# Kernel tuning notes

Hardware: AMD Instinct MI355X
Metric: run time of the kernel (lower is better)

The kernel has to match this reference:

```python
import jax, jax.numpy as jnp
import numpy as np

N_LAYERS = 200
KSIZE = 7
L_IN = 1388
FC_IN = 188   # 1388 - 200*6
FC_OUT = 91


def setup_inputs() -> dict:
    key = jax.random.key(0)
    k_x, k_w, k_b, k_fw, k_fb = jax.random.split(key, 5)
    B = 1024
    x = jax.random.normal(k_x, (B, L_IN), dtype=jnp.float32)
    # Conv1d(1,1,7) weights: torch default init U(-s, s) with s = 1/sqrt(in_ch*k) = 1/sqrt(7)
    s = 1.0 / np.sqrt(KSIZE)
    conv_w = jax.random.uniform(k_w, (N_LAYERS, KSIZE), dtype=jnp.float32, minval=-s, maxval=s)
    conv_b = jax.random.uniform(k_b, (N_LAYERS,), dtype=jnp.float32, minval=-s, maxval=s)
    sf = 1.0 / np.sqrt(FC_IN)
    fc_w = jax.random.uniform(k_fw, (FC_OUT, FC_IN), dtype=jnp.float32, minval=-sf, maxval=sf)
    fc_b = jax.random.uniform(k_fb, (FC_OUT,), dtype=jnp.float32, minval=-sf, maxval=sf)
    return {"x": x, "conv_w": conv_w, "conv_b": conv_b, "fc_w": fc_w, "fc_b": fc_b}


def _conv1(h, w, b):
    # h: [B, L]; cross-correlation with taps w[0..6], valid padding -> [B, L-6]
    L_out = h.shape[1] - (KSIZE - 1)
    acc = w[0] * h[:, 0:L_out]
    for k in range(1, KSIZE):
        acc = acc + w[k] * h[:, k:k + L_out]
    return acc + b


def reference(x, conv_w, conv_b, fc_w, fc_b):
    h = x  # unsqueeze(1) is implicit: single channel handled as [B, L]
    for i in range(N_LAYERS):
        h = _conv1(h, conv_w[i], conv_b[i])
        if i < N_LAYERS - 1:  # last ReLU was popped in the torch module
            h = jax.nn.relu(h)
    # Linear(188, 91) applied to the length dim, then Sigmoid; squeeze channel dim
    out = jax.nn.sigmoid(h @ fc_w.T + fc_b)  # [B, 91]
    return out
```

## Files before the change

### kernel.cpp

```cpp
#include <hip/hip_runtime.h>
#include <math.h>

#define N_LAYERS 200
#define KSIZE 7
#define L_IN 1388
#define FC_IN 188
#define FC_OUT 91
#define NT 128
#define NSTAGES 13

typedef float v2f __attribute__((ext_vector_type(2)));

constexpr int s_lo(int s)  { return 16 * s; }
constexpr int s_hi(int s)  { return (s < 12) ? 16 * s + 16 : N_LAYERS; }
constexpr int lin_(int s)  { return L_IN - 6 * s_lo(s); }
constexpr int lout_(int s) { return L_IN - 6 * s_hi(s); }
constexpr int cut_(int s)  { return lout_(s) / 2; }
constexpr int marg_(int s) { return 6 * (s_hi(s) - s_lo(s)); }
constexpr int s_R(int s) {
    const int a = cut_(s) + marg_(s);
    const int b = lin_(s) - cut_(s);
    const int m = (a > b) ? a : b;
    return (m + 63) / 64;
}
constexpr int s_Re(int s) { return (s_R(s) + 1) & ~1; }

__device__ __forceinline__ float dpp_next(float v) {
    return __int_as_float(
        __builtin_amdgcn_mov_dpp(__float_as_int(v), 0x130, 0xf, 0xf, true));
}
__device__ __forceinline__ v2f dpp_next2(v2f v) {
    v2f o; o.x = dpp_next(v.x); o.y = dpp_next(v.y); return o;
}

__device__ __forceinline__ v2f pk_fma(v2f a, v2f b, v2f c) {
    return __builtin_elementwise_fma(a, b, c);
}
__device__ __forceinline__ v2f pk_max0(v2f a) {
    return __builtin_elementwise_max(a, (v2f)(0.0f));
}

struct WG { v2f w2[28]; v2f b2[4]; };

__device__ __forceinline__ void load_wg(WG& wg, const v2f* wbuf2,
                                        const v2f* bbuf2, int g) {
#pragma unroll
    for (int t = 0; t < 28; ++t) wg.w2[t] = wbuf2[g * 28 + t];
#pragma unroll
    for (int j = 0; j < 4; ++j) wg.b2[j] = bbuf2[g * 4 + j];
}

template<int R, bool NR3>
__device__ __forceinline__ void run4(v2f (&r2)[6], const WG& wg) {
    constexpr int P = R / 2;
#pragma unroll
    for (int jj = 0; jj < 4; ++jj) {
        v2f h[3];
        {
            constexpr int L1 = (P < 3) ? P : 3;
            v2f l1[L1];
#pragma unroll
            for (int t = 0; t < L1; ++t) l1[t] = dpp_next2(r2[t]);
#pragma unroll
            for (int t = 0; t < L1; ++t) h[t] = l1[t];
            if constexpr (P == 2) h[2] = dpp_next2(l1[0]);
        }
        v2f M[P + 2];
#pragma unroll
        for (int j = 0; j < P + 2; ++j) {
            const v2f a = (j < P) ? r2[j] : h[j - P];
            const v2f b = (j + 1 < P) ? r2[j + 1] : h[j + 1 - P];
            v2f m; m.x = a.y; m.y = b.x;
            M[j] = m;
        }
        const bool relu = !(NR3 && jj == 3);
#pragma unroll
        for (int j = 0; j < P; ++j) {
            v2f acc = wg.b2[jj];
#pragma unroll
            for (int d = 0; d < KSIZE; ++d) {
                v2f src;
                if (d % 2 == 0) {
                    const int m = j + d / 2;
                    src = (m < P) ? r2[m] : h[m - P];
                } else {
                    src = M[j + (d - 1) / 2];
                }
                acc = pk_fma(wg.w2[jj * 7 + d], src, acc);
            }
            r2[j] = relu ? pk_max0(acc) : acc;
        }
    }
}

template<int R, bool FINAL>
__device__ __forceinline__ void run_stage_g(v2f (&r2)[6], WG& A,
        const v2f* wbuf2, const v2f* bbuf2, int g0, int g1) {
#pragma unroll 1
    for (int g = g0; g < g1; g += 2) {
        WG B;
        load_wg(B, wbuf2, bbuf2, (g + 1 < 50) ? g + 1 : 49);
        run4<R, false>(r2, A);
        load_wg(A, wbuf2, bbuf2, (g + 2 < 50) ? g + 2 : 49);
        run4<R, FINAL>(r2, B);
    }
}

template<int Ro, int Rn>
__device__ __forceinline__ void repack(v2f (&r2)[6], v2f* lbuf2,
                                       int lane, int wid,
                                       int cut_o, int lout_o, int cut_n)
{
    const int base2  = (wid ? cut_o : 0) / 2;
    const int bound2 = (wid ? lout_o : cut_o) / 2;
#pragma unroll
    for (int j = 0; j < Ro / 2; ++j) {
        const int pg = base2 + lane * (Ro / 2) + j;
        if (pg < bound2) lbuf2[pg] = r2[j];
    }
    __syncthreads();
    const int nb2 = (wid ? cut_n : 0) / 2;
#pragma unroll
    for (int j = 0; j < Rn / 2; ++j) r2[j] = lbuf2[nb2 + lane * (Rn / 2) + j];
    __syncthreads();
}

template<int S>
struct Chain {
    __device__ static __forceinline__ void run(v2f (&r2)[6], WG& A,
        const v2f* wbuf2, const v2f* bbuf2, v2f* lbuf2, int lane, int wid)
    {
        run_stage_g<s_Re(S), false>(r2, A, wbuf2, bbuf2, 4 * S, 4 * S + 4);
        repack<s_Re(S), s_Re(S + 1)>(r2, lbuf2, lane, wid,
                                     cut_(S), lout_(S), cut_(S + 1));
        Chain<S + 1>::run(r2, A, wbuf2, bbuf2, lbuf2, lane, wid);
    }
};

template<>
struct Chain<NSTAGES - 1> {
    __device__ static __forceinline__ void run(v2f (&r2)[6], WG& A,
        const v2f* wbuf2, const v2f* bbuf2, v2f* lbuf2, int lane, int wid)
    {
        constexpr int R = s_Re(NSTAGES - 1);
        run_stage_g<R, true>(r2, A, wbuf2, bbuf2, 48, 50);
        const int base2  = wid ? 47 : 0;
        const int bound2 = wid ? 94 : 47;
#pragma unroll
        for (int j = 0; j < R / 2; ++j) {
            const int pg = base2 + lane * (R / 2) + j;
            if (pg < bound2) lbuf2[pg] = r2[j];
        }
        __syncthreads();
    }
};

__global__ __launch_bounds__(NT, 2) void conv_chain_kernel(
    const float* __restrict__ x,
    const float* __restrict__ conv_w,
    const float* __restrict__ conv_b,
    const float* __restrict__ fc_w,
    const float* __restrict__ fc_b,
    float* __restrict__ out)
{
    __shared__ __align__(16) v2f lbuf2[688];
    __shared__ __align__(16) v2f wbuf2[N_LAYERS * KSIZE];
    __shared__ __align__(16) v2f bbuf2[N_LAYERS];

    const int row  = blockIdx.x;
    const int tid  = threadIdx.x;
    const int lane = tid & 63;
    const int wid  = tid >> 6;

    for (int i = tid; i < N_LAYERS * KSIZE; i += NT) {
        const float v = conv_w[i];
        v2f p; p.x = v; p.y = v; wbuf2[i] = p;
    }
    for (int i = tid; i < N_LAYERS; i += NT) {
        const float v = conv_b[i];
        v2f p; p.x = v; p.y = v; bbuf2[i] = p;
    }

    v2f r2[6];
    const float* xr = x + (size_t)row * L_IN;
    const int c0 = wid ? cut_(0) : 0;
#pragma unroll
    for (int j = 0; j < 6; ++j) {
        const int p = c0 + lane * 12 + 2 * j;
        v2f v;
        if (p + 1 < L_IN)      v = *(const v2f*)(xr + p);
        else if (p < L_IN)     { v.x = xr[p]; v.y = 0.0f; }
        else                   { v.x = 0.0f;  v.y = 0.0f; }
        r2[j] = v;
    }
    __syncthreads();

    WG A;
    load_wg(A, wbuf2, bbuf2, 0);

    Chain<0>::run(r2, A, wbuf2, bbuf2, lbuf2, lane, wid);

    if (tid < FC_OUT) {
        float acc = fc_b[tid];
        const float4* wp = (const float4*)(fc_w + tid * FC_IN);
        const float4* hp = (const float4*)lbuf2;
#pragma unroll 4
        for (int q = 0; q < FC_IN / 4; ++q) {
            const float4 hv = hp[q];
            const float4 wv = wp[q];
            acc = fmaf(wv.x, hv.x, acc);
            acc = fmaf(wv.y, hv.y, acc);
            acc = fmaf(wv.z, hv.z, acc);
            acc = fmaf(wv.w, hv.w, acc);
        }
        out[(size_t)row * FC_OUT + tid] = 1.0f / (1.0f + expf(-acc));
    }
}

extern "C" void kernel_launch(void* const* d_in, const int* in_sizes, int n_in,
                              void* d_out, int out_size, void* d_ws, size_t ws_size,
                              hipStream_t stream) {
    const float* x      = (const float*)d_in[0];
    const float* conv_w = (const float*)d_in[1];
    const float* conv_b = (const float*)d_in[2];
    const float* fc_w   = (const float*)d_in[3];
    const float* fc_b   = (const float*)d_in[4];
    float* outp = (float*)d_out;

    const int batch = in_sizes[0] / L_IN;
    conv_chain_kernel<<<batch, NT, 0, stream>>>(x, conv_w, conv_b, fc_w, fc_b, outp);
}
```

Baseline: 115.3 us.

## Split each row across four waves with scalar FMAs and packed weight buffer

Each row is now processed by four wavefronts (256 threads) instead of two, with each lane holding up to 7 scalar values rather than packed float2 pairs, so the per-lane serial conv chain is shorter. Weights and biases are stored interleaved in one shared buffer of 32 floats per 4-layer group and loaded as float4. Launch bounds request 4 blocks per SU-equivalent. It trades packed FMA throughput and more halo recomputation and barrier participants for more parallel waves per row and lower per-lane latency.

```diff
diff --git a/kernel.cpp b/kernel.cpp
--- a/kernel.cpp
+++ b/kernel.cpp
@@ -6,156 +6,120 @@
 #define L_IN 1388
 #define FC_IN 188
 #define FC_OUT 91
-#define NT 128
+#define NT 256
+#define NW 4
 #define NSTAGES 13
+#define NGROUPS 50
+#define LBUF_N 1352
 
-typedef float v2f __attribute__((ext_vector_type(2)));
-
-constexpr int s_lo(int s)  { return 16 * s; }
-constexpr int s_hi(int s)  { return (s < 12) ? 16 * s + 16 : N_LAYERS; }
-constexpr int lin_(int s)  { return L_IN - 6 * s_lo(s); }
-constexpr int lout_(int s) { return L_IN - 6 * s_hi(s); }
-constexpr int cut_(int s)  { return lout_(s) / 2; }
-constexpr int marg_(int s) { return 6 * (s_hi(s) - s_lo(s)); }
+constexpr int lin_(int s)  { return L_IN - 96 * s; }
+constexpr int lout_(int s) { return (s < 12) ? L_IN - 96 * (s + 1) : FC_IN; }
+constexpr int nlay_(int s) { return (s < 12) ? 16 : 8; }
 constexpr int s_R(int s) {
-    const int a = cut_(s) + marg_(s);
-    const int b = lin_(s) - cut_(s);
-    const int m = (a > b) ? a : b;
-    return (m + 63) / 64;
+    const int span = lout_(s) / 4 + 1 + 6 * nlay_(s);
+    return (span + 63) / 64;
 }
-constexpr int s_Re(int s) { return (s_R(s) + 1) & ~1; }
 
 __device__ __forceinline__ float dpp_next(float v) {
     return __int_as_float(
         __builtin_amdgcn_mov_dpp(__float_as_int(v), 0x130, 0xf, 0xf, true));
 }
-__device__ __forceinline__ v2f dpp_next2(v2f v) {
-    v2f o; o.x = dpp_next(v.x); o.y = dpp_next(v.y); return o;
-}
 
-__device__ __forceinline__ v2f pk_fma(v2f a, v2f b, v2f c) {
-    return __builtin_elementwise_fma(a, b, c);
-}
-__device__ __forceinline__ v2f pk_max0(v2f a) {
-    return __builtin_elementwise_max(a, (v2f)(0.0f));
-}
+struct __align__(16) WG { float w[32]; };
 
-struct WG { v2f w2[28]; v2f b2[4]; };
-
-__device__ __forceinline__ void load_wg(WG& wg, const v2f* wbuf2,
-                                        const v2f* bbuf2, int g) {
+__device__ __forceinline__ void load_wg(WG& wg, const float4* kb4, int g) {
 #pragma unroll
-    for (int t = 0; t < 28; ++t) wg.w2[t] = wbuf2[g * 28 + t];
-#pragma unroll
-    for (int j = 0; j < 4; ++j) wg.b2[j] = bbuf2[g * 4 + j];
+    for (int q = 0; q < 8; ++q)
+        *reinterpret_cast<float4*>(&wg.w[4 * q]) = kb4[g * 8 + q];
 }
 
 template<int R, bool NR3>
-__device__ __forceinline__ void run4(v2f (&r2)[6], const WG& wg) {
-    constexpr int P = R / 2;
+__device__ __forceinline__ void run4(float (&r)[7], const WG& wg) {
 #pragma unroll
     for (int jj = 0; jj < 4; ++jj) {
-        v2f h[3];
+        float h[6];
         {
-            constexpr int L1 = (P < 3) ? P : 3;
-            v2f l1[L1];
+            constexpr int H1 = (R < 6) ? R : 6;
 #pragma unroll
-            for (int t = 0; t < L1; ++t) l1[t] = dpp_next2(r2[t]);
+            for (int t = 0; t < H1; ++t) h[t] = dpp_next(r[t]);
 #pragma unroll
-            for (int t = 0; t < L1; ++t) h[t] = l1[t];
-            if constexpr (P == 2) h[2] = dpp_next2(l1[0]);
-        }
-        v2f M[P + 2];
-#pragma unroll
-        for (int j = 0; j < P + 2; ++j) {
-            const v2f a = (j < P) ? r2[j] : h[j - P];
-            const v2f b = (j + 1 < P) ? r2[j + 1] : h[j + 1 - P];
-            v2f m; m.x = a.y; m.y = b.x;
-            M[j] = m;
+            for (int t = H1; t < 6; ++t) h[t] = dpp_next(h[t - R]);
         }
         const bool relu = !(NR3 && jj == 3);
 #pragma unroll
-        for (int j = 0; j < P; ++j) {
-            v2f acc = wg.b2[jj];
+        for (int j = 0; j < R; ++j) {
+            float acc = wg.w[28 + jj];
 #pragma unroll
             for (int d = 0; d < KSIZE; ++d) {
-                v2f src;
-                if (d % 2 == 0) {
-                    const int m = j + d / 2;
-                    src = (m < P) ? r2[m] : h[m - P];
-                } else {
-                    src = M[j + (d - 1) / 2];
-                }
-                acc = pk_fma(wg.w2[jj * 7 + d], src, acc);
+                const int m = j + d;
+                const float src = (m < R) ? r[m] : h[m - R];
+                acc = fmaf(wg.w[jj * 7 + d], src, acc);
             }
-            r2[j] = relu ? pk_max0(acc) : acc;
+            r[j] = relu ? fmaxf(acc, 0.0f) : acc;
         }
     }
 }
 
 template<int R, bool FINAL>
-__device__ __forceinline__ void run_stage_g(v2f (&r2)[6], WG& A,
-        const v2f* wbuf2, const v2f* bbuf2, int g0, int g1) {
+__device__ __forceinline__ void run_stage_g(float (&r)[7], WG& A,
+        const float4* kb4, int g0, int g1) {
 #pragma unroll 1
     for (int g = g0; g < g1; g += 2) {
         WG B;
-        load_wg(B, wbuf2, bbuf2, (g + 1 < 50) ? g + 1 : 49);
-        run4<R, false>(r2, A);
-        load_wg(A, wbuf2, bbuf2, (g + 2 < 50) ? g + 2 : 49);
-        run4<R, FINAL>(r2, B);
+        load_wg(B, kb4, (g + 1 < NGROUPS) ? g + 1 : NGROUPS - 1);
+        run4<R, false>(r, A);
+        load_wg(A, kb4, (g + 2 < NGROUPS) ? g + 2 : NGROUPS - 1);
+        run4<R, FINAL>(r, B);
     }
 }
 
 template<int Ro, int Rn>
-__device__ __forceinline__ void repack(v2f (&r2)[6], v2f* lbuf2,
-                                       int lane, int wid,
-                                       int cut_o, int lout_o, int cut_n)
-{
-    const int base2  = (wid ? cut_o : 0) / 2;
-    const int bound2 = (wid ? lout_o : cut_o) / 2;
+__device__ __forceinline__ void repack(float (&r)[7], float* lbuf,
+                                       int lane, int co, int co1, int cn) {
 #pragma unroll
-    for (int j = 0; j < Ro / 2; ++j) {
-        const int pg = base2 + lane * (Ro / 2) + j;
-        if (pg < bound2) lbuf2[pg] = r2[j];
+    for (int j = 0; j < Ro; ++j) {
+        const int p = co + lane * Ro + j;
+        if (p < co1) lbuf[p] = r[j];
     }
     __syncthreads();
-    const int nb2 = (wid ? cut_n : 0) / 2;
 #pragma unroll
-    for (int j = 0; j < Rn / 2; ++j) r2[j] = lbuf2[nb2 + lane * (Rn / 2) + j];
+    for (int j = 0; j < Rn; ++j) r[j] = lbuf[cn + lane * Rn + j];
     __syncthreads();
 }
 
 template<int S>
 struct Chain {
-    __device__ static __forceinline__ void run(v2f (&r2)[6], WG& A,
-        const v2f* wbuf2, const v2f* bbuf2, v2f* lbuf2, int lane, int wid)
+    __device__ static __forceinline__ void run(float (&r)[7], WG& A,
+        const float4* kb4, float* lbuf, int lane, int wid)
     {
-        run_stage_g<s_Re(S), false>(r2, A, wbuf2, bbuf2, 4 * S, 4 * S + 4);
-        repack<s_Re(S), s_Re(S + 1)>(r2, lbuf2, lane, wid,
-                                     cut_(S), lout_(S), cut_(S + 1));
-        Chain<S + 1>::run(r2, A, wbuf2, bbuf2, lbuf2, lane, wid);
+        run_stage_g<s_R(S), false>(r, A, kb4, 4 * S, 4 * S + 4);
+        const int co  = (wid * lout_(S)) >> 2;
+        const int co1 = ((wid + 1) * lout_(S)) >> 2;
+        const int cn  = (wid * lout_(S + 1)) >> 2;
+        repack<s_R(S), s_R(S + 1)>(r, lbuf, lane, co, co1, cn);
+        Chain<S + 1>::run(r, A, kb4, lbuf, lane, wid);
     }
 };
 
 template<>
 struct Chain<NSTAGES - 1> {
-    __device__ static __forceinline__ void run(v2f (&r2)[6], WG& A,
-        const v2f* wbuf2, const v2f* bbuf2, v2f* lbuf2, int lane, int wid)
+    __device__ static __forceinline__ void run(float (&r)[7], WG& A,
+        const float4* kb4, float* lbuf, int lane, int wid)
     {
-        constexpr int R = s_Re(NSTAGES - 1);
-        run_stage_g<R, true>(r2, A, wbuf2, bbuf2, 48, 50);
-        const int base2  = wid ? 47 : 0;
-        const int bound2 = wid ? 94 : 47;
+        constexpr int R = s_R(NSTAGES - 1);
+        run_stage_g<R, true>(r, A, kb4, 48, 50);
+        const int co  = (wid * FC_IN) >> 2;
+        const int co1 = ((wid + 1) * FC_IN) >> 2;
 #pragma unroll
-        for (int j = 0; j < R / 2; ++j) {
-            const int pg = base2 + lane * (R / 2) + j;
-            if (pg < bound2) lbuf2[pg] = r2[j];
+        for (int j = 0; j < R; ++j) {
+            const int p = co + lane * R + j;
+            if (p < co1) lbuf[p] = r[j];
         }
         __syncthreads();
     }
 };
 
-__global__ __launch_bounds__(NT, 2) void conv_chain_kernel(
+__global__ __launch_bounds__(NT, 4) void conv_chain_kernel(
     const float* __restrict__ x,
     const float* __restrict__ conv_w,
     const float* __restrict__ conv_b,
@@ -163,47 +127,40 @@
     const float* __restrict__ fc_b,
     float* __restrict__ out)
 {
-    __shared__ __align__(16) v2f lbuf2[688];
-    __shared__ __align__(16) v2f wbuf2[N_LAYERS * KSIZE];
-    __shared__ __align__(16) v2f bbuf2[N_LAYERS];
+    __shared__ __align__(16) float lbuf[LBUF_N];
+    __shared__ __align__(16) float kbuf[NGROUPS * 32];
 
     const int row  = blockIdx.x;
     const int tid  = threadIdx.x;
     const int lane = tid & 63;
     const int wid  = tid >> 6;
 
-    for (int i = tid; i < N_LAYERS * KSIZE; i += NT) {
-        const float v = conv_w[i];
-        v2f p; p.x = v; p.y = v; wbuf2[i] = p;
+    for (int i = tid; i < NGROUPS * 32; i += NT) {
+        const int g = i >> 5, t = i & 31;
+        kbuf[i] = (t < 28) ? conv_w[g * 28 + t] : conv_b[g * 4 + (t - 28)];
     }
-    for (int i = tid; i < N_LAYERS; i += NT) {
-        const float v = conv_b[i];
-        v2f p; p.x = v; p.y = v; bbuf2[i] = p;
-    }
+    for (int i = tid; i < LBUF_N; i += NT) lbuf[i] = 0.0f;
 
-    v2f r2[6];
+    float r[7];
     const float* xr = x + (size_t)row * L_IN;
-    const int c0 = wid ? cut_(0) : 0;
+    const int c0 = (wid * lout_(0)) >> 2;
 #pragma unroll
-    for (int j = 0; j < 6; ++j) {
-        const int p = c0 + lane * 12 + 2 * j;
-        v2f v;
-        if (p + 1 < L_IN)      v = *(const v2f*)(xr + p);
-        else if (p < L_IN)     { v.x = xr[p]; v.y = 0.0f; }
-        else                   { v.x = 0.0f;  v.y = 0.0f; }
-        r2[j] = v;
+    for (int j = 0; j < 7; ++j) {
+        const int p = c0 + lane * 7 + j;
+        r[j] = (p < L_IN) ? xr[p] : 0.0f;
     }
     __syncthreads();
 
     WG A;
-    load_wg(A, wbuf2, bbuf2, 0);
+    const float4* kb4 = reinterpret_cast<const float4*>(kbuf);
+    load_wg(A, kb4, 0);
 
-    Chain<0>::run(r2, A, wbuf2, bbuf2, lbuf2, lane, wid);
+    Chain<0>::run(r, A, kb4, lbuf, lane, wid);
 
     if (tid < FC_OUT) {
         float acc = fc_b[tid];
         const float4* wp = (const float4*)(fc_w + tid * FC_IN);
-        const float4* hp = (const float4*)lbuf2;
+        const float4* hp = (const float4*)lbuf;
 #pragma unroll 4
         for (int q = 0; q < FC_IN / 4; ++q) {
             const float4 hv = hp[q];
```

Result: slower. 132.6 us (+15.0%).

## Process two batch rows per block with 256 threads sharing weight LDS

Applied to the files above, without the earlier changes.

Each block now handles two rows using four waves (two per row), with separate LDS repack buffers per row, and launches half as many blocks. This amortizes the per-block weight/bias staging into shared memory across two rows and halves block count. In exchange, the block-wide syncthreads now couple two rows, so their stalls overlap less freely. Launch bounds stay at (NT,2), which may raise register pressure limits and change occupancy. Batch must be even.

```diff
diff --git a/kernel.cpp b/kernel.cpp
--- a/kernel.cpp
+++ b/kernel.cpp
@@ -6,7 +6,7 @@
 #define L_IN 1388
 #define FC_IN 188
 #define FC_OUT 91
-#define NT 128
+#define NT 256
 #define NSTAGES 13
 
 typedef float v2f __attribute__((ext_vector_type(2)));
@@ -108,18 +108,18 @@
 
 template<int Ro, int Rn>
 __device__ __forceinline__ void repack(v2f (&r2)[6], v2f* lbuf2,
-                                       int lane, int wid,
+                                       int lane, int rwid,
                                        int cut_o, int lout_o, int cut_n)
 {
-    const int base2  = (wid ? cut_o : 0) / 2;
-    const int bound2 = (wid ? lout_o : cut_o) / 2;
+    const int base2  = (rwid ? cut_o : 0) / 2;
+    const int bound2 = (rwid ? lout_o : cut_o) / 2;
 #pragma unroll
     for (int j = 0; j < Ro / 2; ++j) {
         const int pg = base2 + lane * (Ro / 2) + j;
         if (pg < bound2) lbuf2[pg] = r2[j];
     }
     __syncthreads();
-    const int nb2 = (wid ? cut_n : 0) / 2;
+    const int nb2 = (rwid ? cut_n : 0) / 2;
 #pragma unroll
     for (int j = 0; j < Rn / 2; ++j) r2[j] = lbuf2[nb2 + lane * (Rn / 2) + j];
     __syncthreads();
@@ -128,24 +128,24 @@
 template<int S>
 struct Chain {
     __device__ static __forceinline__ void run(v2f (&r2)[6], WG& A,
-        const v2f* wbuf2, const v2f* bbuf2, v2f* lbuf2, int lane, int wid)
+        const v2f* wbuf2, const v2f* bbuf2, v2f* lbuf2, int lane, int rwid)
     {
         run_stage_g<s_Re(S), false>(r2, A, wbuf2, bbuf2, 4 * S, 4 * S + 4);
-        repack<s_Re(S), s_Re(S + 1)>(r2, lbuf2, lane, wid,
+        repack<s_Re(S), s_Re(S + 1)>(r2, lbuf2, lane, rwid,
                                      cut_(S), lout_(S), cut_(S + 1));
-        Chain<S + 1>::run(r2, A, wbuf2, bbuf2, lbuf2, lane, wid);
+        Chain<S + 1>::run(r2, A, wbuf2, bbuf2, lbuf2, lane, rwid);
     }
 };
 
 template<>
 struct Chain<NSTAGES - 1> {
     __device__ static __forceinline__ void run(v2f (&r2)[6], WG& A,
-        const v2f* wbuf2, const v2f* bbuf2, v2f* lbuf2, int lane, int wid)
+        const v2f* wbuf2, const v2f* bbuf2, v2f* lbuf2, int lane, int rwid)
     {
         constexpr int R = s_Re(NSTAGES - 1);
         run_stage_g<R, true>(r2, A, wbuf2, bbuf2, 48, 50);
-        const int base2  = wid ? 47 : 0;
-        const int bound2 = wid ? 94 : 47;
+        const int base2  = rwid ? 47 : 0;
+        const int bound2 = rwid ? 94 : 47;
 #pragma unroll
         for (int j = 0; j < R / 2; ++j) {
             const int pg = base2 + lane * (R / 2) + j;
@@ -163,14 +163,18 @@
     const float* __restrict__ fc_b,
     float* __restrict__ out)
 {
-    __shared__ __align__(16) v2f lbuf2[688];
+    __shared__ __align__(16) v2f lbuf2[2][688];
     __shared__ __align__(16) v2f wbuf2[N_LAYERS * KSIZE];
     __shared__ __align__(16) v2f bbuf2[N_LAYERS];
 
-    const int row  = blockIdx.x;
-    const int tid  = threadIdx.x;
-    const int lane = tid & 63;
-    const int wid  = tid >> 6;
+    const int tid   = threadIdx.x;
+    const int lane  = tid & 63;
+    const int wid   = tid >> 6;
+    const int rsel  = wid >> 1;
+    const int rwid  = wid & 1;
+    const int row   = blockIdx.x * 2 + rsel;
+
+    v2f* lbufr = lbuf2[rsel];
 
     for (int i = tid; i < N_LAYERS * KSIZE; i += NT) {
         const float v = conv_w[i];
@@ -183,7 +187,7 @@
 
     v2f r2[6];
     const float* xr = x + (size_t)row * L_IN;
-    const int c0 = wid ? cut_(0) : 0;
+    const int c0 = rwid ? cut_(0) : 0;
 #pragma unroll
     for (int j = 0; j < 6; ++j) {
         const int p = c0 + lane * 12 + 2 * j;
@@ -198,12 +202,13 @@
     WG A;
     load_wg(A, wbuf2, bbuf2, 0);
 
-    Chain<0>::run(r2, A, wbuf2, bbuf2, lbuf2, lane, wid);
-
-    if (tid < FC_OUT) {
-        float acc = fc_b[tid];
-        const float4* wp = (const float4*)(fc_w + tid * FC_IN);
-        const float4* hp = (const float4*)lbuf2;
+    Chain<0>::run(r2, A, wbuf2, bbuf2, lbufr, lane, rwid);
+
+    const int pt = tid & 127;
+    if (pt < FC_OUT) {
+        float acc = fc_b[pt];
+        const float4* wp = (const float4*)(fc_w + pt * FC_IN);
+        const float4* hp = (const float4*)lbufr;
 #pragma unroll 4
         for (int q = 0; q < FC_IN / 4; ++q) {
             const float4 hv = hp[q];
@@ -213,7 +218,7 @@
             acc = fmaf(wv.z, hv.z, acc);
             acc = fmaf(wv.w, hv.w, acc);
         }
-        out[(size_t)row * FC_OUT + tid] = 1.0f / (1.0f + expf(-acc));
+        out[(size_t)row * FC_OUT + pt] = 1.0f / (1.0f + expf(-acc));
     }
 }
 
@@ -228,5 +233,5 @@
     float* outp = (float*)d_out;
 
     const int batch = in_sizes[0] / L_IN;
-    conv_chain_kernel<<<batch, NT, 0, stream>>>(x, conv_w, conv_b, fc_w, fc_b, outp);
-}
+    conv_chain_kernel<<<batch / 2, NT, 0, stream>>>(x, conv_w, conv_b, fc_w, fc_b, outp);
+}
```

Measured after the change: 113.6 us. Within noise of the previous version (-1.5%).

## Split each row across four wavefronts instead of two

Applied to the files above, without the earlier changes.

Doubles the block to 256 threads and divides each row's sequence into four per-wave segments, each with its own halo margin. Each lane now holds at most 8 elements instead of 12, so the per-wave work in the 200-layer conv chain is roughly halved. The cost is more redundant halo computation across waves, a repack sync involving four waves, and extra shared-memory zeroing. Launch bounds now request 4 blocks per SM so occupancy can keep up.

```diff
diff --git a/kernel.cpp b/kernel.cpp
--- a/kernel.cpp
+++ b/kernel.cpp
@@ -6,23 +6,27 @@
 #define L_IN 1388
 #define FC_IN 188
 #define FC_OUT 91
-#define NT 128
+#define NT 256
 #define NSTAGES 13
 
 typedef float v2f __attribute__((ext_vector_type(2)));
 
 constexpr int s_lo(int s)  { return 16 * s; }
 constexpr int s_hi(int s)  { return (s < 12) ? 16 * s + 16 : N_LAYERS; }
-constexpr int lin_(int s)  { return L_IN - 6 * s_lo(s); }
 constexpr int lout_(int s) { return L_IN - 6 * s_hi(s); }
-constexpr int cut_(int s)  { return lout_(s) / 2; }
 constexpr int marg_(int s) { return 6 * (s_hi(s) - s_lo(s)); }
-constexpr int s_R(int s) {
-    const int a = cut_(s) + marg_(s);
-    const int b = lin_(s) - cut_(s);
-    const int m = (a > b) ? a : b;
-    return (m + 63) / 64;
-}
+constexpr int cutw(int s, int w) {
+    return (w >= 4) ? lout_(s) : ((w * lout_(s)) / 4) & ~1;
+}
+constexpr int maxspan_(int s) {
+    int m = 0;
+    for (int w = 0; w < 4; ++w) {
+        const int sp = cutw(s, w + 1) - cutw(s, w);
+        if (sp > m) m = sp;
+    }
+    return m;
+}
+constexpr int s_R(int s)  { return (maxspan_(s) + marg_(s) + 63) / 64; }
 constexpr int s_Re(int s) { return (s_R(s) + 1) & ~1; }
 
 __device__ __forceinline__ float dpp_next(float v) {
@@ -51,19 +55,17 @@
 }
 
 template<int R, bool NR3>
-__device__ __forceinline__ void run4(v2f (&r2)[6], const WG& wg) {
+__device__ __forceinline__ void run4(v2f (&r2)[4], const WG& wg) {
     constexpr int P = R / 2;
 #pragma unroll
     for (int jj = 0; jj < 4; ++jj) {
         v2f h[3];
         {
             constexpr int L1 = (P < 3) ? P : 3;
-            v2f l1[L1];
-#pragma unroll
-            for (int t = 0; t < L1; ++t) l1[t] = dpp_next2(r2[t]);
-#pragma unroll
-            for (int t = 0; t < L1; ++t) h[t] = l1[t];
-            if constexpr (P == 2) h[2] = dpp_next2(l1[0]);
+#pragma unroll
+            for (int t = 0; t < L1; ++t) h[t] = dpp_next2(r2[t]);
+#pragma unroll
+            for (int t = L1; t < 3; ++t) h[t] = dpp_next2(h[t - P]);
         }
         v2f M[P + 2];
 #pragma unroll
@@ -94,7 +96,7 @@
 }
 
 template<int R, bool FINAL>
-__device__ __forceinline__ void run_stage_g(v2f (&r2)[6], WG& A,
+__device__ __forceinline__ void run_stage_g(v2f (&r2)[4], WG& A,
         const v2f* wbuf2, const v2f* bbuf2, int g0, int g1) {
 #pragma unroll 1
     for (int g = g0; g < g1; g += 2) {
@@ -107,19 +109,17 @@
 }
 
 template<int Ro, int Rn>
-__device__ __forceinline__ void repack(v2f (&r2)[6], v2f* lbuf2,
-                                       int lane, int wid,
-                                       int cut_o, int lout_o, int cut_n)
-{
-    const int base2  = (wid ? cut_o : 0) / 2;
-    const int bound2 = (wid ? lout_o : cut_o) / 2;
+__device__ __forceinline__ void repack(v2f (&r2)[4], v2f* lbuf2,
+                                       int lane, int co, int co1, int cn) {
+    const int base2  = co / 2;
+    const int bound2 = co1 / 2;
 #pragma unroll
     for (int j = 0; j < Ro / 2; ++j) {
         const int pg = base2 + lane * (Ro / 2) + j;
         if (pg < bound2) lbuf2[pg] = r2[j];
     }
     __syncthreads();
-    const int nb2 = (wid ? cut_n : 0) / 2;
+    const int nb2 = cn / 2;
 #pragma unroll
     for (int j = 0; j < Rn / 2; ++j) r2[j] = lbuf2[nb2 + lane * (Rn / 2) + j];
     __syncthreads();
@@ -127,25 +127,26 @@
 
 template<int S>
 struct Chain {
-    __device__ static __forceinline__ void run(v2f (&r2)[6], WG& A,
+    __device__ static __forceinline__ void run(v2f (&r2)[4], WG& A,
         const v2f* wbuf2, const v2f* bbuf2, v2f* lbuf2, int lane, int wid)
     {
         run_stage_g<s_Re(S), false>(r2, A, wbuf2, bbuf2, 4 * S, 4 * S + 4);
-        repack<s_Re(S), s_Re(S + 1)>(r2, lbuf2, lane, wid,
-                                     cut_(S), lout_(S), cut_(S + 1));
+        repack<s_Re(S), s_Re(S + 1)>(r2, lbuf2, lane,
+                                     cutw(S, wid), cutw(S, wid + 1),
+                                     cutw(S + 1, wid));
         Chain<S + 1>::run(r2, A, wbuf2, bbuf2, lbuf2, lane, wid);
     }
 };
 
 template<>
 struct Chain<NSTAGES - 1> {
-    __device__ static __forceinline__ void run(v2f (&r2)[6], WG& A,
+    __device__ static __forceinline__ void run(v2f (&r2)[4], WG& A,
         const v2f* wbuf2, const v2f* bbuf2, v2f* lbuf2, int lane, int wid)
     {
         constexpr int R = s_Re(NSTAGES - 1);
         run_stage_g<R, true>(r2, A, wbuf2, bbuf2, 48, 50);
-        const int base2  = wid ? 47 : 0;
-        const int bound2 = wid ? 94 : 47;
+        const int base2  = cutw(NSTAGES - 1, wid) / 2;
+        const int bound2 = cutw(NSTAGES - 1, wid + 1) / 2;
 #pragma unroll
         for (int j = 0; j < R / 2; ++j) {
             const int pg = base2 + lane * (R / 2) + j;
@@ -155,7 +156,7 @@
     }
 };
 
-__global__ __launch_bounds__(NT, 2) void conv_chain_kernel(
+__global__ __launch_bounds__(NT, 4) void conv_chain_kernel(
     const float* __restrict__ x,
     const float* __restrict__ conv_w,
     const float* __restrict__ conv_b,
@@ -163,7 +164,7 @@
     const float* __restrict__ fc_b,
     float* __restrict__ out)
 {
-    __shared__ __align__(16) v2f lbuf2[688];
+    __shared__ __align__(16) v2f lbuf2[704];
     __shared__ __align__(16) v2f wbuf2[N_LAYERS * KSIZE];
     __shared__ __align__(16) v2f bbuf2[N_LAYERS];
 
@@ -180,13 +181,16 @@
         const float v = conv_b[i];
         v2f p; p.x = v; p.y = v; bbuf2[i] = p;
     }
-
-    v2f r2[6];
+    for (int i = tid; i < 704; i += NT) {
+        v2f z; z.x = 0.0f; z.y = 0.0f; lbuf2[i] = z;
+    }
+
+    v2f r2[4];
     const float* xr = x + (size_t)row * L_IN;
-    const int c0 = wid ? cut_(0) : 0;
-#pragma unroll
-    for (int j = 0; j < 6; ++j) {
-        const int p = c0 + lane * 12 + 2 * j;
+    const int c0 = cutw(0, wid);
+#pragma unroll
+    for (int j = 0; j < 4; ++j) {
+        const int p = c0 + lane * 8 + 2 * j;
         v2f v;
         if (p + 1 < L_IN)      v = *(const v2f*)(xr + p);
         else if (p < L_IN)     { v.x = xr[p]; v.y = 0.0f; }
```

Measured after the change: 162.7 us. 41.1% more time.
